# Kernel optimization log

Measured on AMD Instinct MI355X. Metric: run time of the kernel, lower is better.

Reference implementation:

```python
import jax, jax.numpy as jnp
import numpy as np

B, T, D = 4, 2048, 1024
H = 16
HD = D // H

def setup_inputs() -> dict:
    key = jax.random.key(0)
    k1, k2, k3, k4, k5 = jax.random.split(key, 5)
    x = jax.random.normal(k1, (B, T, D), dtype=jnp.float32)
    scale = 1.0 / np.sqrt(D)
    W_qkv = jax.random.normal(k2, (D, 3 * D), dtype=jnp.float32) * scale
    b_qkv = jnp.zeros((3 * D,), dtype=jnp.float32)
    W_proj = jax.random.normal(k3, (D, D), dtype=jnp.float32) * scale
    b_proj = jnp.zeros((D,), dtype=jnp.float32)
    return {"x": x, "W_qkv": W_qkv, "b_qkv": b_qkv, "W_proj": W_proj, "b_proj": b_proj}

def reference(x, W_qkv, b_qkv, W_proj, b_proj):
    Bx, Tx, C = x.shape
    qkv = x @ W_qkv + b_qkv                      # [B,T,3C]
    q, k, v = jnp.split(qkv, 3, axis=-1)
    # [B,T,H,hd] -> [B,H,T,hd]
    q = q.reshape(Bx, Tx, H, HD).transpose(0, 2, 1, 3)
    k = k.reshape(Bx, Tx, H, HD).transpose(0, 2, 1, 3)
    v = v.reshape(Bx, Tx, H, HD).transpose(0, 2, 1, 3)
    att = jnp.einsum('bhqd,bhkd->bhqk', q, k) / jnp.sqrt(jnp.float32(HD))
    causal = jnp.tril(jnp.ones((Tx, Tx), dtype=bool))
    att = jnp.where(causal[None, None], att, -jnp.inf)
    att = jax.nn.softmax(att, axis=-1)
    y = jnp.einsum('bhqk,bhkd->bhqd', att, v)    # [B,H,T,hd]
    y = y.transpose(0, 2, 1, 3).reshape(Bx, Tx, C)
    return y @ W_proj + b_proj
```

## Files before the change

kernel.cpp:

```cpp
#include <hip/hip_runtime.h>
#include <hip/hip_bf16.h>

#define B_  4
#define T_  2048
#define D_  1024
#define H_  16
#define HD_ 64

typedef short s16x8 __attribute__((ext_vector_type(8)));
typedef short s16x4 __attribute__((ext_vector_type(4)));
typedef float f32x4 __attribute__((ext_vector_type(4)));
typedef unsigned int u32x2 __attribute__((ext_vector_type(2)));

#define MFMA32(a, b, c) __builtin_amdgcn_mfma_f32_16x16x32_bf16(a, b, c, 0, 0, 0)
#define MFMA16(a, b, c) __builtin_amdgcn_mfma_f32_16x16x16bf16_1k(a, b, c, 0, 0, 0)

__device__ __forceinline__ unsigned short f2bf(float f) {
  unsigned u = __builtin_bit_cast(unsigned, f);
  u += 0x7fffu + ((u >> 16) & 1u);
  return (unsigned short)(u >> 16);
}

__device__ __forceinline__ float bf2f(unsigned short h) {
  return __builtin_bit_cast(float, (unsigned)h << 16);
}

#define GLOAD_LDS16(src, dst)                                            \
  __builtin_amdgcn_global_load_lds(                                      \
      (__attribute__((address_space(1))) void*)(void*)(src),             \
      (__attribute__((address_space(3))) void*)(dst), 16, 0, 0)

__global__ __launch_bounds__(256) void convert_x_kernel(
    const float* __restrict__ in, unsigned short* __restrict__ out, int n8) {
  int i = blockIdx.x * 256 + threadIdx.x;
  if (i >= n8) return;
  const float4* p = ((const float4*)in) + (size_t)i * 2;
  float4 a = p[0], b = p[1];
  s16x8 o;
  o[0] = (short)f2bf(a.x); o[1] = (short)f2bf(a.y);
  o[2] = (short)f2bf(a.z); o[3] = (short)f2bf(a.w);
  o[4] = (short)f2bf(b.x); o[5] = (short)f2bf(b.y);
  o[6] = (short)f2bf(b.z); o[7] = (short)f2bf(b.w);
  *(((s16x8*)out) + i) = o;
}

__global__ __launch_bounds__(256) void transpose_w_kernel(
    const float* __restrict__ W, unsigned short* __restrict__ Wt, int K, int N) {
  __shared__ float tile[32][33];
  int n0 = blockIdx.x * 32, k0 = blockIdx.y * 32;
  int tx = threadIdx.x & 31, ty = threadIdx.x >> 5;
#pragma unroll
  for (int j = 0; j < 4; ++j) {
    int k = ty + j * 8;
    tile[k][tx] = W[(size_t)(k0 + k) * N + n0 + tx];
  }
  __syncthreads();
#pragma unroll
  for (int j = 0; j < 4; ++j) {
    int n = ty + j * 8;
    Wt[(size_t)(n0 + n) * K + k0 + tx] = f2bf(tile[tx][n]);
  }
}

template <int OUTF32>
__global__ __launch_bounds__(256) void gemm_kernel(
    const unsigned short* __restrict__ A, const unsigned short* __restrict__ Bt,
    const float* __restrict__ bias, void* __restrict__ Cout, int M, int N, int K) {
  __shared__ char lds[32768];
  char* Al = lds;
  char* Bl = lds + 16384;
  const int n0 = blockIdx.x * 128, m0 = blockIdx.y * 128;
  const int w = threadIdx.x >> 6, lane = threadIdx.x & 63;
  const int l15 = lane & 15, g = lane >> 4;
  const int wr = w >> 1, wc = w & 1;
  const int srow = (lane >> 3);
  const int u = lane & 7;
  f32x4 acc[4][4] = {};

  for (int kt = 0; kt < K; kt += 64) {
    __syncthreads();
#pragma unroll
    for (int i = 0; i < 4; ++i) {
      int c = w * 4 + i;
      int row = c * 8 + srow;
      const unsigned short* srcA = A + (size_t)(m0 + row) * K + kt + u * 8;
      GLOAD_LDS16(srcA, Al + c * 1024);
      const unsigned short* srcB = Bt + (size_t)(n0 + row) * K + kt + u * 8;
      GLOAD_LDS16(srcB, Bl + c * 1024);
    }
    __syncthreads();
#pragma unroll
    for (int kk = 0; kk < 2; ++kk) {
      s16x8 af[4], bfr[4];
#pragma unroll
      for (int mi = 0; mi < 4; ++mi) {
        int row = wr * 64 + mi * 16 + l15;
        af[mi] = *(const s16x8*)(Al + row * 128 + kk * 64 + g * 16);
      }
#pragma unroll
      for (int ni = 0; ni < 4; ++ni) {
        int row = wc * 64 + ni * 16 + l15;
        bfr[ni] = *(const s16x8*)(Bl + row * 128 + kk * 64 + g * 16);
      }
#pragma unroll
      for (int mi = 0; mi < 4; ++mi)
#pragma unroll
        for (int ni = 0; ni < 4; ++ni)
          acc[mi][ni] = MFMA32(af[mi], bfr[ni], acc[mi][ni]);
    }
  }
#pragma unroll
  for (int ni = 0; ni < 4; ++ni) {
    int col = n0 + wc * 64 + ni * 16 + l15;
    float bv = bias[col];
#pragma unroll
    for (int mi = 0; mi < 4; ++mi) {
      int row = m0 + wr * 64 + mi * 16 + g * 4;
#pragma unroll
      for (int r = 0; r < 4; ++r) {
        float v = acc[mi][ni][r] + bv;
        if (OUTF32)
          ((float*)Cout)[(size_t)(row + r) * N + col] = v;
        else
          ((unsigned short*)Cout)[(size_t)(row + r) * N + col] = f2bf(v);
      }
    }
  }
}

__global__ __launch_bounds__(256, 4) void attn_kernel(
    const unsigned short* __restrict__ qkv, unsigned short* __restrict__ yatt) {
  __shared__ char lds[8192 + 9344];
  const int bx = blockIdx.x;
  const int bh = blockIdx.y;
  const int b = bh >> 4, h = bh & 15;
  const int w = threadIdx.x >> 6;
  const int lane = threadIdx.x & 63;
  const int l15 = lane & 15, g = lane >> 4;

  const size_t rowstride = 3 * D_;
  const unsigned short* Qb = qkv + (size_t)b * T_ * rowstride + h * HD_;
  const unsigned short* Kb = Qb + D_;
  const unsigned short* Vb = Qb + 2 * D_;

  char* Klds = lds;
  unsigned short* Vt = (unsigned short*)(lds + 8192);

  const int krow0 = (w * 2 + 0) * 8 + (lane >> 3);
  const int krow1 = (w * 2 + 1) * 8 + (lane >> 3);
  const int u = lane & 7;
  const int vkey = w * 16 + (lane >> 2);
  const int vdb = lane & 3;
  const float SC = 0.18033688011112042f;

  const int qtA = 31 - bx;
  const int nA = qtA + 1;

  s16x8 kc0, kc1, vc0, vc1;
  s16x8 kn0, kn1, vn0, vn1;

  auto ld = [&](int kt, s16x8& a, s16x8& b2, s16x8& c, s16x8& d2) {
    const unsigned short* kb = Kb + (size_t)(kt * 64) * rowstride;
    a = *(const s16x8*)(kb + (size_t)krow0 * rowstride + u * 8);
    b2 = *(const s16x8*)(kb + (size_t)krow1 * rowstride + u * 8);
    const unsigned short* vs = Vb + (size_t)(kt * 64 + vkey) * rowstride + vdb * 16;
    c = *(const s16x8*)(vs);
    d2 = *(const s16x8*)(vs + 8);
  };

  ld(0, kc0, kc1, vc0, vc1);
  ld(1, kn0, kn1, vn0, vn1);
  int f = 0;

#pragma unroll 1
  for (int ti = 0; ti < 2; ++ti) {
    const int qt = ti ? bx : qtA;
    s16x8 qf0, qf1;
    {
      const unsigned short* qr = Qb + (size_t)(qt * 64 + w * 16 + l15) * rowstride;
      s16x8 a0 = *(const s16x8*)(qr + g * 8);
      s16x8 a1 = *(const s16x8*)(qr + 32 + g * 8);
#pragma unroll
      for (int j = 0; j < 8; ++j) {
        qf0[j] = (short)f2bf(bf2f((unsigned short)a0[j]) * SC);
        qf1[j] = (short)f2bf(bf2f((unsigned short)a1[j]) * SC);
      }
    }
    float m = -1e30f, rs = 0.f;
    f32x4 acc[4] = {};

#pragma unroll 1
    for (int kt = 0; kt <= qt; ++kt) {
      __syncthreads();
      *(s16x8*)(Klds + krow0 * 128 + ((u ^ (krow0 & 7)) << 4)) = kc0;
      *(s16x8*)(Klds + krow1 * 128 + ((u ^ (krow1 & 7)) << 4)) = kc1;
#pragma unroll
      for (int j = 0; j < 8; ++j) {
        Vt[vdb * 1168 + j * 72 + vkey] = (unsigned short)vc0[j];
        Vt[vdb * 1168 + (8 + j) * 72 + vkey] = (unsigned short)vc1[j];
      }
      __syncthreads();
      kc0 = kn0; kc1 = kn1; vc0 = vn0; vc1 = vn1;
      {
        int f2 = f + 2;
        if (f2 < 33) {
          int kt2 = (f2 < nA) ? f2 : f2 - nA;
          ld(kt2, kn0, kn1, vn0, vn1);
        }
      }

      float tv[16];
      __builtin_amdgcn_s_setprio(1);
#pragma unroll
      for (int kk = 0; kk < 4; ++kk) {
        int key = kk * 16 + l15;
        const s16x8 kf0 = *(const s16x8*)(Klds + key * 128 + ((g ^ (key & 7)) << 4));
        const s16x8 kf1 = *(const s16x8*)(Klds + key * 128 + (((4 + g) ^ (key & 7)) << 4));
        f32x4 s = {};
        s = MFMA32(kf0, qf0, s);
        s = MFMA32(kf1, qf1, s);
#pragma unroll
        for (int r = 0; r < 4; ++r) tv[kk * 4 + r] = s[r];
      }
      __builtin_amdgcn_s_setprio(0);
      if (kt == qt) {
        int q = qt * 64 + w * 16 + l15;
#pragma unroll
        for (int kk = 0; kk < 4; ++kk)
#pragma unroll
          for (int r = 0; r < 4; ++r)
            if (kt * 64 + kk * 16 + g * 4 + r > q) tv[kk * 4 + r] = -1e30f;
      }
      float x0 = fmaxf(tv[0], tv[1]), x1 = fmaxf(tv[2], tv[3]);
      float x2 = fmaxf(tv[4], tv[5]), x3 = fmaxf(tv[6], tv[7]);
      float x4 = fmaxf(tv[8], tv[9]), x5 = fmaxf(tv[10], tv[11]);
      float x6 = fmaxf(tv[12], tv[13]), x7 = fmaxf(tv[14], tv[15]);
      float tm = fmaxf(fmaxf(fmaxf(x0, x1), fmaxf(x2, x3)),
                       fmaxf(fmaxf(x4, x5), fmaxf(x6, x7)));
      tm = fmaxf(tm, __shfl_xor(tm, 16));
      tm = fmaxf(tm, __shfl_xor(tm, 32));
      if (!__all(tm - m <= 8.0f)) {
        float mn = fmaxf(m, tm);
        float corr = exp2f(m - mn);
        m = mn;
        rs *= corr;
#pragma unroll
        for (int i = 0; i < 4; ++i) {
          acc[i][0] *= corr; acc[i][1] *= corr;
          acc[i][2] *= corr; acc[i][3] *= corr;
        }
      }
      s16x4 pb[4];
      float ps = 0.f;
#pragma unroll
      for (int kk = 0; kk < 4; ++kk) {
        float p0 = exp2f(tv[kk * 4 + 0] - m), p1 = exp2f(tv[kk * 4 + 1] - m);
        float p2 = exp2f(tv[kk * 4 + 2] - m), p3 = exp2f(tv[kk * 4 + 3] - m);
        ps += (p0 + p1) + (p2 + p3);
        u32x2 pk;
        pk[0] = __builtin_amdgcn_perm(__builtin_bit_cast(unsigned, p1),
                                      __builtin_bit_cast(unsigned, p0), 0x07060302u);
        pk[1] = __builtin_amdgcn_perm(__builtin_bit_cast(unsigned, p3),
                                      __builtin_bit_cast(unsigned, p2), 0x07060302u);
        pb[kk] = __builtin_bit_cast(s16x4, pk);
      }
      rs += ps;
      __builtin_amdgcn_s_setprio(1);
#pragma unroll
      for (int kk = 0; kk < 4; ++kk) {
#pragma unroll
        for (int db = 0; db < 4; ++db) {
          s16x4 vf = *(const s16x4*)(Vt + db * 1168 + l15 * 72 + kk * 16 + g * 4);
          acc[db] = MFMA16(vf, pb[kk], acc[db]);
        }
      }
      __builtin_amdgcn_s_setprio(0);
      ++f;
    }

    float rtot = rs + __shfl_xor(rs, 16);
    rtot += __shfl_xor(rtot, 32);
    float inv = 1.0f / rtot;
    __syncthreads();
    unsigned short* ylds = (unsigned short*)lds;
#pragma unroll
    for (int db = 0; db < 4; ++db)
#pragma unroll
      for (int r = 0; r < 4; ++r)
        ylds[(db * 16 + g * 4 + r) * 66 + w * 16 + l15] = f2bf(acc[db][r] * inv);
    __syncthreads();
    int qq = threadIdx.x >> 2;
    int dc = (threadIdx.x & 3) * 16;
    s16x8 o1, o2;
#pragma unroll
    for (int j = 0; j < 8; ++j) {
      o1[j] = (short)ylds[(dc + j) * 66 + qq];
      o2[j] = (short)ylds[(dc + 8 + j) * 66 + qq];
    }
    unsigned short* dst = yatt + (size_t)(b * T_ + qt * 64 + qq) * D_ + h * HD_ + dc;
    *(s16x8*)(dst) = o1;
    *(s16x8*)(dst + 8) = o2;
  }
}

extern "C" void kernel_launch(void* const* d_in, const int* in_sizes, int n_in,
                              void* d_out, int out_size, void* d_ws, size_t ws_size,
                              hipStream_t stream) {
  const float* x     = (const float*)d_in[0];
  const float* Wqkv  = (const float*)d_in[1];
  const float* bqkv  = (const float*)d_in[2];
  const float* Wproj = (const float*)d_in[3];
  const float* bproj = (const float*)d_in[4];
  float* out = (float*)d_out;

  unsigned short* xb   = (unsigned short*)d_ws;
  unsigned short* Wqb  = xb + (size_t)8192 * 1024;
  unsigned short* Wpb  = Wqb + (size_t)3072 * 1024;
  unsigned short* qkvb = Wpb + (size_t)1024 * 1024;
  unsigned short* yb   = xb;

  convert_x_kernel<<<dim3(4096), dim3(256), 0, stream>>>(x, xb, 8192 * 1024 / 8);
  transpose_w_kernel<<<dim3(96, 32), dim3(256), 0, stream>>>(Wqkv, Wqb, 1024, 3072);
  transpose_w_kernel<<<dim3(32, 32), dim3(256), 0, stream>>>(Wproj, Wpb, 1024, 1024);
  gemm_kernel<0><<<dim3(24, 64), dim3(256), 0, stream>>>(xb, Wqb, bqkv, qkvb, 8192, 3072, 1024);
  attn_kernel<<<dim3(16, 64), dim3(256), 0, stream>>>(qkvb, yb);
  gemm_kernel<1><<<dim3(8, 64), dim3(256), 0, stream>>>(yb, Wpb, bproj, out, 8192, 1024, 1024);
}
```

Baseline: 210.8 us.

## Compute softmax row sums via MFMA, swizzle GEMM blocks, repad V tile

The attention kernel now takes the softmax denominator from an extra MFMA that multiplies the bf16 probabilities by a ones vector. This replaces the scalar fp32 adds and the cross-lane shuffle reduction. The sum is now built from the bf16-rounded probabilities, which matches the numerator but changes rounding slightly. The transposed V LDS tile stride goes from 72 to 76 to change bank mapping, the max reduction is regrouped into fmax3-friendly triples, and GEMM workgroup ids are remapped so that consecutive blocks spread across eight chunks.

```diff
diff --git a/kernel.cpp b/kernel.cpp
--- a/kernel.cpp
+++ b/kernel.cpp
@@ -69,7 +69,10 @@
   __shared__ char lds[32768];
   char* Al = lds;
   char* Bl = lds + 16384;
-  const int n0 = blockIdx.x * 128, m0 = blockIdx.y * 128;
+  int lid = blockIdx.y * gridDim.x + blockIdx.x;
+  int chunk = (gridDim.x * gridDim.y) >> 3;
+  int swz = (lid & 7) * chunk + (lid >> 3);
+  const int n0 = (swz % gridDim.x) * 128, m0 = (swz / gridDim.x) * 128;
   const int w = threadIdx.x >> 6, lane = threadIdx.x & 63;
   const int l15 = lane & 15, g = lane >> 4;
   const int wr = w >> 1, wc = w & 1;
@@ -128,9 +131,11 @@
   }
 }
 
+#define VT_STR 76
+#define VT_BLK 1232
 __global__ __launch_bounds__(256, 4) void attn_kernel(
     const unsigned short* __restrict__ qkv, unsigned short* __restrict__ yatt) {
-  __shared__ char lds[8192 + 9344];
+  __shared__ char lds[8192 + 4 * VT_BLK * 2];
   const int bx = blockIdx.x;
   const int bh = blockIdx.y;
   const int b = bh >> 4, h = bh & 15;
@@ -152,6 +157,7 @@
   const int vkey = w * 16 + (lane >> 2);
   const int vdb = lane & 3;
   const float SC = 0.18033688011112042f;
+  const s16x4 onesf = {(short)0x3F80, (short)0x3F80, (short)0x3F80, (short)0x3F80};
 
   const int qtA = 31 - bx;
   const int nA = qtA + 1;
@@ -186,8 +192,9 @@
         qf1[j] = (short)f2bf(bf2f((unsigned short)a1[j]) * SC);
       }
     }
-    float m = -1e30f, rs = 0.f;
+    float m = -1e30f;
     f32x4 acc[4] = {};
+    f32x4 accS = {};
 
 #pragma unroll 1
     for (int kt = 0; kt <= qt; ++kt) {
@@ -196,8 +203,8 @@
       *(s16x8*)(Klds + krow1 * 128 + ((u ^ (krow1 & 7)) << 4)) = kc1;
 #pragma unroll
       for (int j = 0; j < 8; ++j) {
-        Vt[vdb * 1168 + j * 72 + vkey] = (unsigned short)vc0[j];
-        Vt[vdb * 1168 + (8 + j) * 72 + vkey] = (unsigned short)vc1[j];
+        Vt[vdb * VT_BLK + j * VT_STR + vkey] = (unsigned short)vc0[j];
+        Vt[vdb * VT_BLK + (8 + j) * VT_STR + vkey] = (unsigned short)vc1[j];
       }
       __syncthreads();
       kc0 = kn0; kc1 = kn1; vc0 = vn0; vc1 = vn1;
@@ -231,32 +238,32 @@
           for (int r = 0; r < 4; ++r)
             if (kt * 64 + kk * 16 + g * 4 + r > q) tv[kk * 4 + r] = -1e30f;
       }
-      float x0 = fmaxf(tv[0], tv[1]), x1 = fmaxf(tv[2], tv[3]);
-      float x2 = fmaxf(tv[4], tv[5]), x3 = fmaxf(tv[6], tv[7]);
-      float x4 = fmaxf(tv[8], tv[9]), x5 = fmaxf(tv[10], tv[11]);
-      float x6 = fmaxf(tv[12], tv[13]), x7 = fmaxf(tv[14], tv[15]);
-      float tm = fmaxf(fmaxf(fmaxf(x0, x1), fmaxf(x2, x3)),
-                       fmaxf(fmaxf(x4, x5), fmaxf(x6, x7)));
+      float a0 = fmaxf(fmaxf(tv[0], tv[1]), tv[2]);
+      float a1 = fmaxf(fmaxf(tv[3], tv[4]), tv[5]);
+      float a2 = fmaxf(fmaxf(tv[6], tv[7]), tv[8]);
+      float a3 = fmaxf(fmaxf(tv[9], tv[10]), tv[11]);
+      float a4 = fmaxf(fmaxf(tv[12], tv[13]), tv[14]);
+      float b0 = fmaxf(fmaxf(a0, a1), a2);
+      float b1 = fmaxf(fmaxf(a3, a4), tv[15]);
+      float tm = fmaxf(b0, b1);
       tm = fmaxf(tm, __shfl_xor(tm, 16));
       tm = fmaxf(tm, __shfl_xor(tm, 32));
       if (!__all(tm - m <= 8.0f)) {
         float mn = fmaxf(m, tm);
         float corr = exp2f(m - mn);
         m = mn;
-        rs *= corr;
 #pragma unroll
         for (int i = 0; i < 4; ++i) {
           acc[i][0] *= corr; acc[i][1] *= corr;
           acc[i][2] *= corr; acc[i][3] *= corr;
         }
+        accS[0] *= corr; accS[1] *= corr; accS[2] *= corr; accS[3] *= corr;
       }
       s16x4 pb[4];
-      float ps = 0.f;
 #pragma unroll
       for (int kk = 0; kk < 4; ++kk) {
         float p0 = exp2f(tv[kk * 4 + 0] - m), p1 = exp2f(tv[kk * 4 + 1] - m);
         float p2 = exp2f(tv[kk * 4 + 2] - m), p3 = exp2f(tv[kk * 4 + 3] - m);
-        ps += (p0 + p1) + (p2 + p3);
         u32x2 pk;
         pk[0] = __builtin_amdgcn_perm(__builtin_bit_cast(unsigned, p1),
                                       __builtin_bit_cast(unsigned, p0), 0x07060302u);
@@ -264,23 +271,21 @@
                                       __builtin_bit_cast(unsigned, p2), 0x07060302u);
         pb[kk] = __builtin_bit_cast(s16x4, pk);
       }
-      rs += ps;
       __builtin_amdgcn_s_setprio(1);
 #pragma unroll
       for (int kk = 0; kk < 4; ++kk) {
 #pragma unroll
         for (int db = 0; db < 4; ++db) {
-          s16x4 vf = *(const s16x4*)(Vt + db * 1168 + l15 * 72 + kk * 16 + g * 4);
+          s16x4 vf = *(const s16x4*)(Vt + db * VT_BLK + l15 * VT_STR + kk * 16 + g * 4);
           acc[db] = MFMA16(vf, pb[kk], acc[db]);
         }
+        accS = MFMA16(onesf, pb[kk], accS);
       }
       __builtin_amdgcn_s_setprio(0);
       ++f;
     }
 
-    float rtot = rs + __shfl_xor(rs, 16);
-    rtot += __shfl_xor(rtot, 32);
-    float inv = 1.0f / rtot;
+    float inv = 1.0f / accS[0];
     __syncthreads();
     unsigned short* ylds = (unsigned short*)lds;
 #pragma unroll
```

After: 207.4 us. About the same (-1.6%).
